# Kernel tuning notes

Hardware: AMD Instinct MI355X
Metric: run time of the kernel (lower is better)

The kernel has to match this reference:

```python
import jax, jax.numpy as jnp
import numpy as np

EMBED = 64
OUT = 64
KERW = 64
DIM = 3

def setup_inputs() -> dict:
    key = jax.random.key(0)
    ks = jax.random.split(key, 6)
    x = jax.random.normal(ks[0], (8, 4096, EMBED), dtype=jnp.float32)
    grid = jax.random.uniform(ks[1], (8, 4096, DIM), dtype=jnp.float32)
    # DenseNet([dim, ker_width_l, output_size*embed_size], GELU): two Linear layers,
    # GELU between, no activation after the last layer.
    W1 = jax.random.normal(ks[2], (DIM, KERW), dtype=jnp.float32) / np.sqrt(DIM)
    b1 = jnp.zeros((KERW,), dtype=jnp.float32)
    W2 = jax.random.normal(ks[3], (KERW, OUT * EMBED), dtype=jnp.float32) / np.sqrt(KERW)
    b2 = jnp.zeros((OUT * EMBED,), dtype=jnp.float32)
    return {"x": x, "grid": grid, "W1": W1, "b1": b1, "W2": W2, "b2": b2}

def reference(x, grid, W1, b1, W2, b2):
    shape = x.shape
    # generator MLP: grid [.., dim] -> per-point weight [.., embed*out]
    h = jax.nn.gelu(grid @ W1 + b1, approximate=False)
    weight = h @ W2 + b2                              # [B, P, embed*out]
    weight = weight.reshape(-1, EMBED, OUT)           # [N, embed, out]
    xf = x.reshape(-1, shape[-1])                     # [N, embed]
    out = jnp.einsum('bi,bio->bo', xf, weight)        # [N, out]
    return out.reshape(*shape[:-1], OUT)
```

## Files before the change

### kernel.cpp

```cpp
#include <hip/hip_runtime.h>
#include <hip/hip_fp16.h>

typedef _Float16 f16x8 __attribute__((ext_vector_type(8)));
typedef float f32x4 __attribute__((ext_vector_type(4)));
typedef float f32x16 __attribute__((ext_vector_type(16)));

#define N_PTS 32768
#define ROWS 64

__global__ __launch_bounds__(256) void prep_kernel(
    const float* __restrict__ W2, const float* __restrict__ b2,
    _Float16* __restrict__ wsB) {
  __shared__ _Float16 w_lds[64][72];
  const int c   = blockIdx.x;
  const int tid = threadIdx.x;
  {
    const float* src = (c < 64) ? (W2 + c * 4096 + tid * 16) : (b2 + tid * 16);
    int kl = tid >> 2, o = (tid & 3) * 16;
    f16x8 v0, v1;
    #pragma unroll
    for (int j = 0; j < 8; ++j) {
      v0[j] = (_Float16)src[j];
      v1[j] = (_Float16)src[8 + j];
    }
    *(f16x8*)(&w_lds[kl][o])     = v0;
    *(f16x8*)(&w_lds[kl][o + 8]) = v1;
  }
  __syncthreads();
  #pragma unroll
  for (int u = 0; u < 2; ++u) {
    int t = tid + u * 256;
    int lane = t & 63;
    int kt   = (t >> 6) & 3;
    int ns   = t >> 8;
    int klbase = kt * 16 + ((lane >> 5) << 3);
    int o      = ns * 32 + (lane & 31);
    f16x8 v;
    #pragma unroll
    for (int j = 0; j < 8; ++j) v[j] = w_lds[klbase + j][o];
    *(f16x8*)(wsB + c * 4096 + t * 8) = v;
  }
}

__global__ __launch_bounds__(256) void main_kernel(
    const float* __restrict__ x, const float* __restrict__ gridp,
    const float* __restrict__ W1, const float* __restrict__ b1,
    const _Float16* __restrict__ wsB, float* __restrict__ out) {

  __shared__ float part[2][ROWS][68];
  __shared__ _Float16 h_t[2][4][ROWS][8];
  _Float16* x_lds = (_Float16*)&part[0][0][0];

  const int tid  = threadIdx.x;
  const int lane = tid & 63;
  const int wave = tid >> 6;
  const int ks   = wave & 1;
  const int ns   = wave >> 1;
  const int rowblk = blockIdx.x * ROWS;
  const int r31 = lane & 31;
  const int hi  = lane >> 5;

  const float* xsrc = x + rowblk * 64 + tid * 16;
  f32x4 xr0 = *(const f32x4*)(xsrc);
  f32x4 xr1 = *(const f32x4*)(xsrc + 4);
  f32x4 xr2 = *(const f32x4*)(xsrc + 8);
  f32x4 xr3 = *(const f32x4*)(xsrc + 12);

  {
    int row = tid >> 2, sub = tid & 3;
    int r = rowblk + row;
    float g0 = gridp[r * 3 + 0], g1 = gridp[r * 3 + 1], g2 = gridp[r * 3 + 2];
    f16x8 he, ho;
    #pragma unroll
    for (int q = 0; q < 16; ++q) {
      int k = sub * 16 + q;
      float v = g0 * W1[k] + g1 * W1[64 + k] + g2 * W1[128 + k] + b1[k];
      float v2 = v * v;
      float pp = fmaf(0.044715f, v2, 1.0f);
      float u  = v * pp;
      float e  = exp2f(u * 2.3022084f);
      float rr = e + 1.0f;
      float inv;
      asm("v_rcp_f32 %0, %1" : "=v"(inv) : "v"(rr));
      float h = v * (1.0f - inv);
      if ((q & 1) == 0) he[q >> 1] = (_Float16)h;
      else              ho[q >> 1] = (_Float16)h;
    }
    *(f16x8*)(&h_t[0][sub][row][0]) = he;
    *(f16x8*)(&h_t[1][sub][row][0]) = ho;
  }

  {
    int row = tid >> 2, o = (tid & 3) * 16;
    f16x8 v0, v1;
    #pragma unroll
    for (int j = 0; j < 4; ++j) {
      v0[j]     = (_Float16)xr0[j];
      v0[4 + j] = (_Float16)xr1[j];
      v1[j]     = (_Float16)xr2[j];
      v1[4 + j] = (_Float16)xr3[j];
    }
    *(f16x8*)(&x_lds[row * 72 + o])     = v0;
    *(f16x8*)(&x_lds[row * 72 + o + 8]) = v1;
  }
  __syncthreads();

  const _Float16* bp = wsB + lane * 8;

  auto LOADB = [&](f16x8* b, int c) {
    #pragma unroll
    for (int kt = 0; kt < 4; ++kt)
      b[kt] = *(const f16x8*)(bp + (c * 8 + ns * 4 + kt) * 512);
  };

  f16x8 bA[4], bB[4], bC[4];
  LOADB(bA, ks);
  LOADB(bB, ks + 2);
  LOADB(bC, ks + 4);

  f16x8 hreg[2][4];
  #pragma unroll
  for (int mt = 0; mt < 2; ++mt)
    #pragma unroll
    for (int ph = 0; ph < 4; ++ph)
      hreg[mt][ph] = *(const f16x8*)(&h_t[ks][ph][mt * 32 + r31][0]);

  f16x8 xf[2][4];
  #pragma unroll
  for (int mt = 0; mt < 2; ++mt)
    #pragma unroll
    for (int kt = 0; kt < 4; ++kt)
      xf[mt][kt] = *(const f16x8*)(&x_lds[(mt * 32 + r31) * 72 + kt * 16 + hi * 8]);

  f32x16 acc[2];
  #pragma unroll
  for (int mt = 0; mt < 2; ++mt)
    #pragma unroll
    for (int i = 0; i < 16; ++i) acc[mt][i] = 0.f;

  auto COMPUTE = [&](const f16x8* b, int p) {
    #pragma unroll
    for (int mt = 0; mt < 2; ++mt) {
      _Float16 hh = hreg[mt][p >> 3][p & 7];
      f16x8 hs = {hh, hh, hh, hh, hh, hh, hh, hh};
      #pragma unroll
      for (int kt = 0; kt < 4; ++kt)
        acc[mt] = __builtin_amdgcn_mfma_f32_32x32x16_f16(xf[mt][kt] * hs, b[kt],
                                                         acc[mt], 0, 0, 0);
    }
  };
  auto COMPUTE_BIAS = [&](const f16x8* b) {
    #pragma unroll
    for (int mt = 0; mt < 2; ++mt)
      #pragma unroll
      for (int kt = 0; kt < 4; ++kt)
        acc[mt] = __builtin_amdgcn_mfma_f32_32x32x16_f16(xf[mt][kt], b[kt],
                                                         acc[mt], 0, 0, 0);
  };

  #pragma unroll
  for (int g = 0; g < 10; ++g) {
    COMPUTE(bA, 3 * g);
    if (3 * g + 3 < 32) LOADB(bA, ks + 2 * (3 * g + 3));
    COMPUTE(bB, 3 * g + 1);
    if (3 * g + 4 < 32) LOADB(bB, ks + 2 * (3 * g + 4));
    COMPUTE(bC, 3 * g + 2);
    if (3 * g + 5 < 32)      LOADB(bC, ks + 2 * (3 * g + 5));
    else if (3 * g + 5 == 32 && ks == 0) LOADB(bC, 64);
  }
  COMPUTE(bA, 30);
  COMPUTE(bB, 31);
  if (ks == 0) COMPUTE_BIAS(bC);

  __syncthreads();

  {
    #pragma unroll
    for (int mt = 0; mt < 2; ++mt)
      #pragma unroll
      for (int r = 0; r < 16; ++r) {
        int rowL = mt * 32 + (r & 3) + 8 * (r >> 2) + 4 * hi;
        part[ks][rowL][ns * 32 + r31] = acc[mt][r];
      }
  }
  __syncthreads();

  {
    int row = tid >> 2;
    int cb  = (tid & 3) * 16;
    float* op = out + (rowblk + row) * 64 + cb;
    #pragma unroll
    for (int j = 0; j < 4; ++j) {
      f32x4 s = *(const f32x4*)(&part[0][row][cb + j * 4]);
      s += *(const f32x4*)(&part[1][row][cb + j * 4]);
      *(f32x4*)(op + j * 4) = s;
    }
  }
}

extern "C" void kernel_launch(void* const* d_in, const int* in_sizes, int n_in,
                              void* d_out, int out_size, void* d_ws, size_t ws_size,
                              hipStream_t stream) {
  const float* x    = (const float*)d_in[0];
  const float* grid = (const float*)d_in[1];
  const float* W1   = (const float*)d_in[2];
  const float* b1   = (const float*)d_in[3];
  const float* W2   = (const float*)d_in[4];
  const float* b2   = (const float*)d_in[5];
  float* out = (float*)d_out;
  _Float16* wsB = (_Float16*)d_ws;

  hipLaunchKernelGGL(prep_kernel, dim3(65), dim3(256), 0, stream,
                     W2, b2, wsB);
  hipLaunchKernelGGL(main_kernel, dim3(N_PTS / ROWS), dim3(256), 0, stream,
                     x, grid, W1, b1, wsB, out);
}
```

Baseline: 32.24 us.

## Split waves by row tile instead of column tile, loading x directly into registers

Each wave now owns one 32-row M tile and both 32-column N tiles, instead of both M tiles and one N tile. The x fragments are loaded straight from global memory into MFMA register layout, which removes the LDS staging round trip for x. The hidden-activation scale multiply is now done once per M tile, where before it was repeated for two tiles. In exchange each wave loads twice as many B fragments per step (8 instead of 4), which raises global/L2 traffic for the weights and register pressure from the triple-buffered B. The GELU layout was also changed to an interleaved h_t and uses the raw exp2 builtin.

Result: slower. 34.43 us (+6.8%).

```diff
diff --git a/kernel.cpp b/kernel.cpp
--- a/kernel.cpp
+++ b/kernel.cpp
@@ -47,115 +47,107 @@
     const float* __restrict__ W1, const float* __restrict__ b1,
     const _Float16* __restrict__ wsB, float* __restrict__ out) {
 
+  __shared__ _Float16 h_t[2][ROWS][36];
   __shared__ float part[2][ROWS][68];
-  __shared__ _Float16 h_t[2][4][ROWS][8];
-  _Float16* x_lds = (_Float16*)&part[0][0][0];
 
   const int tid  = threadIdx.x;
   const int lane = tid & 63;
   const int wave = tid >> 6;
+  const int mg   = wave >> 1;
   const int ks   = wave & 1;
-  const int ns   = wave >> 1;
   const int rowblk = blockIdx.x * ROWS;
   const int r31 = lane & 31;
   const int hi  = lane >> 5;
 
-  const float* xsrc = x + rowblk * 64 + tid * 16;
-  f32x4 xr0 = *(const f32x4*)(xsrc);
-  f32x4 xr1 = *(const f32x4*)(xsrc + 4);
-  f32x4 xr2 = *(const f32x4*)(xsrc + 8);
-  f32x4 xr3 = *(const f32x4*)(xsrc + 12);
+  const float* xr = x + (rowblk + mg * 32 + r31) * 64 + hi * 8;
+  f32x4 xa[4], xb[4];
+  #pragma unroll
+  for (int kt = 0; kt < 4; ++kt) {
+    xa[kt] = *(const f32x4*)(xr + kt * 16);
+    xb[kt] = *(const f32x4*)(xr + kt * 16 + 4);
+  }
 
   {
     int row = tid >> 2, sub = tid & 3;
     int r = rowblk + row;
     float g0 = gridp[r * 3 + 0], g1 = gridp[r * 3 + 1], g2 = gridp[r * 3 + 2];
-    f16x8 he, ho;
-    #pragma unroll
-    for (int q = 0; q < 16; ++q) {
-      int k = sub * 16 + q;
-      float v = g0 * W1[k] + g1 * W1[64 + k] + g2 * W1[128 + k] + b1[k];
-      float v2 = v * v;
-      float pp = fmaf(0.044715f, v2, 1.0f);
-      float u  = v * pp;
-      float e  = exp2f(u * 2.3022084f);
-      float rr = e + 1.0f;
-      float inv;
-      asm("v_rcp_f32 %0, %1" : "=v"(inv) : "v"(rr));
-      float h = v * (1.0f - inv);
-      if ((q & 1) == 0) he[q >> 1] = (_Float16)h;
-      else              ho[q >> 1] = (_Float16)h;
-    }
-    *(f16x8*)(&h_t[0][sub][row][0]) = he;
-    *(f16x8*)(&h_t[1][sub][row][0]) = ho;
-  }
-
-  {
-    int row = tid >> 2, o = (tid & 3) * 16;
-    f16x8 v0, v1;
+    #pragma unroll
+    for (int par = 0; par < 2; ++par) {
+      f16x8 hv;
+      #pragma unroll
+      for (int qq = 0; qq < 8; ++qq) {
+        int k = par + 2 * (sub * 8 + qq);
+        float v = g0 * W1[k] + g1 * W1[64 + k] + g2 * W1[128 + k] + b1[k];
+        float v2 = v * v;
+        float u  = v * fmaf(0.044715f, v2, 1.0f);
+        float e  = __builtin_amdgcn_exp2f(u * 2.3022084f);
+        float rr = e + 1.0f;
+        float inv;
+        asm("v_rcp_f32 %0, %1" : "=v"(inv) : "v"(rr));
+        hv[qq] = (_Float16)(v * (1.0f - inv));
+      }
+      *(f16x8*)(&h_t[par][row][sub * 8]) = hv;
+    }
+  }
+
+  f16x8 xf[4];
+  #pragma unroll
+  for (int kt = 0; kt < 4; ++kt) {
+    f16x8 v;
     #pragma unroll
     for (int j = 0; j < 4; ++j) {
-      v0[j]     = (_Float16)xr0[j];
-      v0[4 + j] = (_Float16)xr1[j];
-      v1[j]     = (_Float16)xr2[j];
-      v1[4 + j] = (_Float16)xr3[j];
-    }
-    *(f16x8*)(&x_lds[row * 72 + o])     = v0;
-    *(f16x8*)(&x_lds[row * 72 + o + 8]) = v1;
+      v[j]     = (_Float16)xa[kt][j];
+      v[4 + j] = (_Float16)xb[kt][j];
+    }
+    xf[kt] = v;
   }
   __syncthreads();
 
   const _Float16* bp = wsB + lane * 8;
-
   auto LOADB = [&](f16x8* b, int c) {
     #pragma unroll
-    for (int kt = 0; kt < 4; ++kt)
-      b[kt] = *(const f16x8*)(bp + (c * 8 + ns * 4 + kt) * 512);
+    for (int q = 0; q < 8; ++q)
+      b[q] = *(const f16x8*)(bp + (c * 8 + q) * 512);
   };
 
-  f16x8 bA[4], bB[4], bC[4];
+  f16x8 bA[8], bB[8], bC[8];
   LOADB(bA, ks);
   LOADB(bB, ks + 2);
   LOADB(bC, ks + 4);
 
-  f16x8 hreg[2][4];
-  #pragma unroll
-  for (int mt = 0; mt < 2; ++mt)
-    #pragma unroll
-    for (int ph = 0; ph < 4; ++ph)
-      hreg[mt][ph] = *(const f16x8*)(&h_t[ks][ph][mt * 32 + r31][0]);
-
-  f16x8 xf[2][4];
-  #pragma unroll
-  for (int mt = 0; mt < 2; ++mt)
-    #pragma unroll
-    for (int kt = 0; kt < 4; ++kt)
-      xf[mt][kt] = *(const f16x8*)(&x_lds[(mt * 32 + r31) * 72 + kt * 16 + hi * 8]);
+  f16x8 hreg[4];
+  #pragma unroll
+  for (int i = 0; i < 4; ++i)
+    hreg[i] = *(const f16x8*)(&h_t[ks][mg * 32 + r31][i * 8]);
 
   f32x16 acc[2];
   #pragma unroll
-  for (int mt = 0; mt < 2; ++mt)
-    #pragma unroll
-    for (int i = 0; i < 16; ++i) acc[mt][i] = 0.f;
+  for (int ns = 0; ns < 2; ++ns)
+    #pragma unroll
+    for (int i = 0; i < 16; ++i) acc[ns][i] = 0.f;
 
   auto COMPUTE = [&](const f16x8* b, int p) {
-    #pragma unroll
-    for (int mt = 0; mt < 2; ++mt) {
-      _Float16 hh = hreg[mt][p >> 3][p & 7];
-      f16x8 hs = {hh, hh, hh, hh, hh, hh, hh, hh};
-      #pragma unroll
-      for (int kt = 0; kt < 4; ++kt)
-        acc[mt] = __builtin_amdgcn_mfma_f32_32x32x16_f16(xf[mt][kt] * hs, b[kt],
-                                                         acc[mt], 0, 0, 0);
-    }
+    _Float16 hh = hreg[p >> 3][p & 7];
+    f16x8 hs = {hh, hh, hh, hh, hh, hh, hh, hh};
+    f16x8 a0 = xf[0] * hs, a1 = xf[1] * hs, a2 = xf[2] * hs, a3 = xf[3] * hs;
+    acc[0] = __builtin_amdgcn_mfma_f32_32x32x16_f16(a0, b[0], acc[0], 0, 0, 0);
+    acc[1] = __builtin_amdgcn_mfma_f32_32x32x16_f16(a0, b[4], acc[1], 0, 0, 0);
+    acc[0] = __builtin_amdgcn_mfma_f32_32x32x16_f16(a1, b[1], acc[0], 0, 0, 0);
+    acc[1] = __builtin_amdgcn_mfma_f32_32x32x16_f16(a1, b[5], acc[1], 0, 0, 0);
+    acc[0] = __builtin_amdgcn_mfma_f32_32x32x16_f16(a2, b[2], acc[0], 0, 0, 0);
+    acc[1] = __builtin_amdgcn_mfma_f32_32x32x16_f16(a2, b[6], acc[1], 0, 0, 0);
+    acc[0] = __builtin_amdgcn_mfma_f32_32x32x16_f16(a3, b[3], acc[0], 0, 0, 0);
+    acc[1] = __builtin_amdgcn_mfma_f32_32x32x16_f16(a3, b[7], acc[1], 0, 0, 0);
   };
   auto COMPUTE_BIAS = [&](const f16x8* b) {
-    #pragma unroll
-    for (int mt = 0; mt < 2; ++mt)
-      #pragma unroll
-      for (int kt = 0; kt < 4; ++kt)
-        acc[mt] = __builtin_amdgcn_mfma_f32_32x32x16_f16(xf[mt][kt], b[kt],
-                                                         acc[mt], 0, 0, 0);
+    acc[0] = __builtin_amdgcn_mfma_f32_32x32x16_f16(xf[0], b[0], acc[0], 0, 0, 0);
+    acc[1] = __builtin_amdgcn_mfma_f32_32x32x16_f16(xf[0], b[4], acc[1], 0, 0, 0);
+    acc[0] = __builtin_amdgcn_mfma_f32_32x32x16_f16(xf[1], b[1], acc[0], 0, 0, 0);
+    acc[1] = __builtin_amdgcn_mfma_f32_32x32x16_f16(xf[1], b[5], acc[1], 0, 0, 0);
+    acc[0] = __builtin_amdgcn_mfma_f32_32x32x16_f16(xf[2], b[2], acc[0], 0, 0, 0);
+    acc[1] = __builtin_amdgcn_mfma_f32_32x32x16_f16(xf[2], b[6], acc[1], 0, 0, 0);
+    acc[0] = __builtin_amdgcn_mfma_f32_32x32x16_f16(xf[3], b[3], acc[0], 0, 0, 0);
+    acc[1] = __builtin_amdgcn_mfma_f32_32x32x16_f16(xf[3], b[7], acc[1], 0, 0, 0);
   };
 
   #pragma unroll
@@ -174,15 +166,13 @@
 
   __syncthreads();
 
-  {
-    #pragma unroll
-    for (int mt = 0; mt < 2; ++mt)
-      #pragma unroll
-      for (int r = 0; r < 16; ++r) {
-        int rowL = mt * 32 + (r & 3) + 8 * (r >> 2) + 4 * hi;
-        part[ks][rowL][ns * 32 + r31] = acc[mt][r];
-      }
-  }
+  #pragma unroll
+  for (int ns = 0; ns < 2; ++ns)
+    #pragma unroll
+    for (int r = 0; r < 16; ++r) {
+      int rowL = mg * 32 + (r & 3) + 8 * (r >> 2) + 4 * hi;
+      part[ks][rowL][ns * 32 + r31] = acc[ns][r];
+    }
   __syncthreads();
 
   {
```
